# Kernel optimization log

Hardware: AMD Instinct MI355X
Metric: run time of the kernel (lower is better)

Reference implementation:

```python
import jax, jax.numpy as jnp
import numpy as np

NUM_GRAPHS = 1024

def setup_inputs() -> dict:
    key = jax.random.key(0)
    ks = jax.random.split(key, 6)
    N, E = 500000, 16000000
    x = jax.random.normal(ks[0], (N, 4), dtype=jnp.float32)
    edge_index = jax.random.randint(ks[1], (2, E), 0, N, dtype=jnp.int32)
    batch = jnp.sort(jax.random.randint(ks[2], (N,), 0, NUM_GRAPHS, dtype=jnp.int32))
    eps = jnp.zeros((), dtype=jnp.float32)
    W1 = jax.random.normal(ks[3], (4, 16), dtype=jnp.float32) * 0.5
    b1 = jnp.zeros((16,), dtype=jnp.float32)
    W2 = jax.random.normal(ks[4], (16, 4), dtype=jnp.float32) * 0.25
    b2 = jnp.zeros((4,), dtype=jnp.float32)
    return {"x": x, "edge_index": edge_index, "batch": batch,
            "eps": eps, "W1": W1, "b1": b1, "W2": W2, "b2": b2}

def reference(x, edge_index, batch, eps, W1, b1, W2, b2):
    N = x.shape[0]
    src, dst = edge_index[0], edge_index[1]
    # GINConv aggregation: sum of neighbor (source) features at each target node
    agg = jax.ops.segment_sum(x[src], dst, num_segments=N)  # [N, 4]
    h = (1.0 + eps) * x + agg
    # 2-layer MLP: Lin(4,16) -> ReLU -> Lin(16,4)
    h = jax.nn.relu(h @ W1 + b1) @ W2 + b2
    h = jax.nn.relu(h)
    # global_mean_pool over batch segment ids
    sums = jax.ops.segment_sum(h, batch, num_segments=NUM_GRAPHS)      # [G, 4]
    cnts = jax.ops.segment_sum(jnp.ones((N,), h.dtype), batch, num_segments=NUM_GRAPHS)
    pooled = sums / jnp.maximum(cnts, 1.0)[:, None]
    return jax.nn.log_softmax(pooled, axis=1)
```

## Files before the change

### kernel.cpp

```cpp
#include <hip/hip_runtime.h>

#define NUM_GRAPHS 1024
#define BIN_BITS 10
#define BIN_SIZE (1 << BIN_BITS)
#define EB 8192
#define STH 512
#define EPT 16
#define ACCTH 256
#define ACCW 4

typedef int v4i __attribute__((ext_vector_type(4)));

__device__ inline unsigned bf16_rn(float f) {
    unsigned u = __float_as_uint(f);
    return (u + 0x7FFFu + ((u >> 16) & 1u)) >> 16;
}
__global__ void prep_kernel(const float4* __restrict__ x, uint2* __restrict__ x16,
                            int N, int* __restrict__ cursor,
                            float* __restrict__ gsum, float* __restrict__ gcnt,
                            int cap) {
    int i = blockIdx.x * blockDim.x + threadIdx.x;
    if (i < 512) cursor[i] = i * cap;
    if (i < NUM_GRAPHS * 4) gsum[i] = 0.0f;
    if (i < NUM_GRAPHS) gcnt[i] = 0.0f;
    if (i < N) {
        float4 v = x[i];
        uint2 r;
        r.x = bf16_rn(v.x) | (bf16_rn(v.y) << 16);
        r.y = bf16_rn(v.z) | (bf16_rn(v.w) << 16);
        x16[i] = r;
    }
}

__global__ void __launch_bounds__(STH) bin_scatter(const int* __restrict__ src,
                                                   const int* __restrict__ dst,
                                                   int* __restrict__ packed,
                                                   int* __restrict__ cursor,
                                                   int E, int cap, int nb) {
    __shared__ int shist[512];
    __shared__ int sprefix[513];
    __shared__ int sgbase[512];
    __shared__ int spacked[EB];
    __shared__ unsigned short sbin[EB];
    __shared__ int wsum[8];

    const int t = threadIdx.x;
    const int lane = t & 63;
    const int wave = t >> 6;
    const int b0 = blockIdx.x * EB;
    const int myBase = b0 + t * EPT;

    for (int j = t; j < 512; j += STH) shist[j] = 0;
    __syncthreads();

    int pv[EPT];
    int bl[EPT];
    const bool full = (myBase + EPT <= E);
    if (full) {
#pragma unroll
        for (int v = 0; v < EPT / 4; ++v) {
            int4 d = *(const int4*)(dst + myBase + v * 4);
            int4 s = *(const int4*)(src + myBase + v * 4);
            int bn, lp;
            bn = ((unsigned)d.x) >> BIN_BITS; lp = atomicAdd(&shist[bn], 1);
            pv[v * 4 + 0] = ((d.x & (BIN_SIZE - 1)) << 19) | s.x;
            bl[v * 4 + 0] = (bn << 13) | lp;
            bn = ((unsigned)d.y) >> BIN_BITS; lp = atomicAdd(&shist[bn], 1);
            pv[v * 4 + 1] = ((d.y & (BIN_SIZE - 1)) << 19) | s.y;
            bl[v * 4 + 1] = (bn << 13) | lp;
            bn = ((unsigned)d.z) >> BIN_BITS; lp = atomicAdd(&shist[bn], 1);
            pv[v * 4 + 2] = ((d.z & (BIN_SIZE - 1)) << 19) | s.z;
            bl[v * 4 + 2] = (bn << 13) | lp;
            bn = ((unsigned)d.w) >> BIN_BITS; lp = atomicAdd(&shist[bn], 1);
            pv[v * 4 + 3] = ((d.w & (BIN_SIZE - 1)) << 19) | s.w;
            bl[v * 4 + 3] = (bn << 13) | lp;
        }
    } else {
#pragma unroll
        for (int i = 0; i < EPT; ++i) {
            int e = myBase + i;
            bool ok = e < E;
            int d = ok ? dst[e] : 0;
            int s = ok ? src[e] : 0;
            int bn = ((unsigned)d) >> BIN_BITS;
            int lp = 0;
            if (ok) lp = atomicAdd(&shist[bn], 1);
            pv[i] = ((d & (BIN_SIZE - 1)) << 19) | s;
            bl[i] = ok ? ((bn << 13) | lp) : -1;
        }
    }
    __syncthreads();

    {
        int v = shist[t];
        int inc = v;
#pragma unroll
        for (int off = 1; off < 64; off <<= 1) {
            int u = __shfl_up(inc, off);
            if (lane >= off) inc += u;
        }
        if (lane == 63) wsum[wave] = inc;
        __syncthreads();
        if (t == 0) {
            int acc = 0;
#pragma unroll
            for (int w = 0; w < 8; ++w) { int c = wsum[w]; wsum[w] = acc; acc += c; }
        }
        __syncthreads();
        sprefix[t + 1] = inc + wsum[wave];
        if (t == 0) sprefix[0] = 0;
        if (t < nb && v > 0) sgbase[t] = atomicAdd(&cursor[t], v);
    }
    __syncthreads();

    if (full) {
#pragma unroll
        for (int i = 0; i < EPT; ++i) {
            int bn = ((unsigned)bl[i]) >> 13;
            int lp = bl[i] & 0x1FFF;
            int idx = sprefix[bn] + lp;
            spacked[idx] = pv[i];
            sbin[idx] = (unsigned short)bn;
        }
    } else {
#pragma unroll
        for (int i = 0; i < EPT; ++i) {
            if (bl[i] >= 0) {
                int bn = ((unsigned)bl[i]) >> 13;
                int lp = bl[i] & 0x1FFF;
                int idx = sprefix[bn] + lp;
                spacked[idx] = pv[i];
                sbin[idx] = (unsigned short)bn;
            }
        }
    }
    __syncthreads();

    int cnt = sprefix[nb < 512 ? nb : 512];
    int totE = E - b0; if (totE < 0) totE = 0;
    if (cnt > totE) cnt = totE;
    for (int j = t; j < cnt; j += STH) {
        int bn = sbin[j];
        int pos = sgbase[bn] + (j - sprefix[bn]);
        if (pos < (bn + 1) * cap)
            __builtin_nontemporal_store(spacked[j], &packed[pos]);
    }
}

__global__ void __launch_bounds__(ACCTH) bin_accum_mlp_pool(
        const float4* __restrict__ x,
        const uint2* __restrict__ x16,
        const int* __restrict__ packed,
        const int* __restrict__ cursor,
        const int* __restrict__ batch,
        const float* __restrict__ eps_p,
        const float* __restrict__ W1, const float* __restrict__ b1,
        const float* __restrict__ W2, const float* __restrict__ b2,
        float* __restrict__ gsum, float* __restrict__ gcnt,
        int N, int cap) {
    __shared__ float planes[ACCW][BIN_SIZE][4];

    const int bin = blockIdx.x;
    const int t = threadIdx.x;
    const int lane = t & 63;
    const int wave = t >> 6;

    {
        float4* pz = (float4*)&planes[0][0][0];
        float4 z; z.x = 0.f; z.y = 0.f; z.z = 0.f; z.w = 0.f;
#pragma unroll
        for (int i = 0; i < 16; ++i) pz[t + i * ACCTH] = z;
    }
    __syncthreads();

    const int start = bin * cap;
    int end = cursor[bin];
    if (end > start + cap) end = start + cap;
    int cnt = end - start; if (cnt < 0) cnt = 0;

    int seg = ((cnt + ACCW - 1) / ACCW + 3) & ~3;
    int s0 = start + wave * seg;
    int s1 = s0 + seg; if (s1 > end) s1 = end;

    for (int base = s0; base < s1; base += 256) {
        int b = base + lane * 4;
        int pe[4];
        if (b + 3 < s1) {
            v4i p4 = __builtin_nontemporal_load((const v4i*)(packed + b));
            pe[0] = p4.x; pe[1] = p4.y; pe[2] = p4.z; pe[3] = p4.w;
        } else {
            pe[0] = (b + 0 < s1) ? packed[b + 0] : -1;
            pe[1] = (b + 1 < s1) ? packed[b + 1] : -1;
            pe[2] = (b + 2 < s1) ? packed[b + 2] : -1;
            pe[3] = (b + 3 < s1) ? packed[b + 3] : -1;
        }
        uint2 g[4];
#pragma unroll
        for (int k = 0; k < 4; ++k) g[k] = x16[pe[k] & 0x7FFFF];

#pragma unroll
        for (int k = 0; k < 4; ++k) {
            int p = pe[k];
            bool ok = p >= 0;
            int dl = (((unsigned)p) >> 19) & (BIN_SIZE - 1);
            unsigned long long m;
            {
                unsigned long long bv = __ballot(ok);
                m = ok ? bv : ~bv;
#pragma unroll
                for (int bb = 0; bb < BIN_BITS; ++bb) {
                    unsigned long long bl_ = __ballot((dl >> bb) & 1);
                    m &= ((dl >> bb) & 1) ? bl_ : ~bl_;
                }
            }
            int rank = ok ? (int)__popcll(m & ((1ull << lane) - 1ull)) : -1;

            float v0 = __uint_as_float(g[k].x << 16);
            float v1 = __uint_as_float(g[k].x & 0xFFFF0000u);
            float v2 = __uint_as_float(g[k].y << 16);
            float v3 = __uint_as_float(g[k].y & 0xFFFF0000u);
            float4* pp = (float4*)&planes[wave][dl][0];
            for (int pass = 0; __any(rank >= pass); ++pass) {
                if (rank == pass) {
                    float4 a = *pp;
                    a.x += v0; a.y += v1; a.z += v2; a.w += v3;
                    *pp = a;
                }
            }
        }
    }
    __syncthreads();

    const float eps = eps_p[0];
    for (int half = 0; half < 4; ++half) {
        int node = t + half * ACCTH;
        float4 a = *(const float4*)&planes[0][node][0];
#pragma unroll
        for (int w = 1; w < ACCW; ++w) {
            float4 bq = *(const float4*)&planes[w][node][0];
            a.x += bq.x; a.y += bq.y; a.z += bq.z; a.w += bq.w;
        }

        int n = bin * BIN_SIZE + node;
        bool valid = n < N;
        float o0 = 0.f, o1 = 0.f, o2 = 0.f, o3 = 0.f;
        int g = -1;
        if (valid) {
            float4 xv = x[n];
            float h0 = (1.0f + eps) * xv.x + a.x;
            float h1 = (1.0f + eps) * xv.y + a.y;
            float h2 = (1.0f + eps) * xv.z + a.z;
            float h3 = (1.0f + eps) * xv.w + a.w;

            float tmp[16];
#pragma unroll
            for (int j = 0; j < 16; ++j) {
                float v = b1[j] + h0 * W1[j] + h1 * W1[16 + j] + h2 * W1[32 + j] + h3 * W1[48 + j];
                tmp[j] = v > 0.0f ? v : 0.0f;
            }
            float o[4];
#pragma unroll
            for (int j = 0; j < 4; ++j) {
                float v = b2[j];
#pragma unroll
                for (int k = 0; k < 16; ++k) v += tmp[k] * W2[k * 4 + j];
                o[j] = v > 0.0f ? v : 0.0f;
            }
            o0 = o[0]; o1 = o[1]; o2 = o[2]; o3 = o[3];
            g = batch[n];
        }

        int g0 = __shfl(g, 0);
        bool uni = __all(g == g0);
        if (uni && g0 >= 0) {
#pragma unroll
            for (int off = 32; off > 0; off >>= 1) {
                o0 += __shfl_down(o0, off);
                o1 += __shfl_down(o1, off);
                o2 += __shfl_down(o2, off);
                o3 += __shfl_down(o3, off);
            }
            if (lane == 0) {
                unsafeAtomicAdd(&gsum[(size_t)g0 * 4 + 0], o0);
                unsafeAtomicAdd(&gsum[(size_t)g0 * 4 + 1], o1);
                unsafeAtomicAdd(&gsum[(size_t)g0 * 4 + 2], o2);
                unsafeAtomicAdd(&gsum[(size_t)g0 * 4 + 3], o3);
                unsafeAtomicAdd(&gcnt[g0], 64.0f);
            }
        } else if (valid) {
            unsafeAtomicAdd(&gsum[(size_t)g * 4 + 0], o0);
            unsafeAtomicAdd(&gsum[(size_t)g * 4 + 1], o1);
            unsafeAtomicAdd(&gsum[(size_t)g * 4 + 2], o2);
            unsafeAtomicAdd(&gsum[(size_t)g * 4 + 3], o3);
            unsafeAtomicAdd(&gcnt[g], 1.0f);
        }
    }
}

__global__ void pool_softmax_kernel(const float* __restrict__ gsum,
                                    const float* __restrict__ gcnt,
                                    float* __restrict__ out) {
    int g = blockIdx.x * blockDim.x + threadIdx.x;
    if (g >= NUM_GRAPHS) return;
    float c = fmaxf(gcnt[g], 1.0f);
    float p0 = gsum[g * 4 + 0] / c;
    float p1 = gsum[g * 4 + 1] / c;
    float p2 = gsum[g * 4 + 2] / c;
    float p3 = gsum[g * 4 + 3] / c;
    float m = fmaxf(fmaxf(p0, p1), fmaxf(p2, p3));
    float s = expf(p0 - m) + expf(p1 - m) + expf(p2 - m) + expf(p3 - m);
    float lse = m + logf(s);
    out[g * 4 + 0] = p0 - lse;
    out[g * 4 + 1] = p1 - lse;
    out[g * 4 + 2] = p2 - lse;
    out[g * 4 + 3] = p3 - lse;
}

__global__ void edge_scatter_kernel(const float4* __restrict__ x,
                                    const int* __restrict__ src,
                                    const int* __restrict__ dst,
                                    float* __restrict__ agg,
                                    int E) {
    int t = blockIdx.x * blockDim.x + threadIdx.x;
    int e = t * 4;
    if (e + 3 < E) {
        int4 s = *(const int4*)(src + e);
        int4 d = *(const int4*)(dst + e);
        float4 xv;
        xv = x[s.x];
        unsafeAtomicAdd(&agg[(size_t)d.x * 4 + 0], xv.x);
        unsafeAtomicAdd(&agg[(size_t)d.x * 4 + 1], xv.y);
        unsafeAtomicAdd(&agg[(size_t)d.x * 4 + 2], xv.z);
        unsafeAtomicAdd(&agg[(size_t)d.x * 4 + 3], xv.w);
        xv = x[s.y];
        unsafeAtomicAdd(&agg[(size_t)d.y * 4 + 0], xv.x);
        unsafeAtomicAdd(&agg[(size_t)d.y * 4 + 1], xv.y);
        unsafeAtomicAdd(&agg[(size_t)d.y * 4 + 2], xv.z);
        unsafeAtomicAdd(&agg[(size_t)d.y * 4 + 3], xv.w);
        xv = x[s.z];
        unsafeAtomicAdd(&agg[(size_t)d.z * 4 + 0], xv.x);
        unsafeAtomicAdd(&agg[(size_t)d.z * 4 + 1], xv.y);
        unsafeAtomicAdd(&agg[(size_t)d.z * 4 + 2], xv.z);
        unsafeAtomicAdd(&agg[(size_t)d.z * 4 + 3], xv.w);
        xv = x[s.w];
        unsafeAtomicAdd(&agg[(size_t)d.w * 4 + 0], xv.x);
        unsafeAtomicAdd(&agg[(size_t)d.w * 4 + 1], xv.y);
        unsafeAtomicAdd(&agg[(size_t)d.w * 4 + 2], xv.z);
        unsafeAtomicAdd(&agg[(size_t)d.w * 4 + 3], xv.w);
    } else {
        for (int i = e; i < E; ++i) {
            int sv = src[i], dv = dst[i];
            float4 xv = x[sv];
            unsafeAtomicAdd(&agg[(size_t)dv * 4 + 0], xv.x);
            unsafeAtomicAdd(&agg[(size_t)dv * 4 + 1], xv.y);
            unsafeAtomicAdd(&agg[(size_t)dv * 4 + 2], xv.z);
            unsafeAtomicAdd(&agg[(size_t)dv * 4 + 3], xv.w);
        }
    }
}

__global__ void node_mlp_pool_kernel(const float4* __restrict__ x,
                                     const float4* __restrict__ agg,
                                     const int* __restrict__ batch,
                                     const float* __restrict__ eps_p,
                                     const float* __restrict__ W1,
                                     const float* __restrict__ b1,
                                     const float* __restrict__ W2,
                                     const float* __restrict__ b2,
                                     float* __restrict__ gsum,
                                     float* __restrict__ gcnt,
                                     int N) {
    int i = blockIdx.x * blockDim.x + threadIdx.x;
    bool valid = i < N;
    float o0 = 0.f, o1 = 0.f, o2 = 0.f, o3 = 0.f;
    int g = -1;
    if (valid) {
        float eps = eps_p[0];
        float4 xv = x[i];
        float4 av = agg[i];
        float h0 = (1.0f + eps) * xv.x + av.x;
        float h1 = (1.0f + eps) * xv.y + av.y;
        float h2 = (1.0f + eps) * xv.z + av.z;
        float h3 = (1.0f + eps) * xv.w + av.w;
        float tmp[16];
#pragma unroll
        for (int j = 0; j < 16; ++j) {
            float v = b1[j] + h0 * W1[j] + h1 * W1[16 + j] + h2 * W1[32 + j] + h3 * W1[48 + j];
            tmp[j] = v > 0.0f ? v : 0.0f;
        }
        float o[4];
#pragma unroll
        for (int j = 0; j < 4; ++j) {
            float v = b2[j];
#pragma unroll
            for (int k = 0; k < 16; ++k) v += tmp[k] * W2[k * 4 + j];
            o[j] = v > 0.0f ? v : 0.0f;
        }
        o0 = o[0]; o1 = o[1]; o2 = o[2]; o3 = o[3];
        g = batch[i];
    }
    int g0 = __shfl(g, 0);
    bool uni = __all(g == g0);
    if (uni && g0 >= 0) {
#pragma unroll
        for (int off = 32; off > 0; off >>= 1) {
            o0 += __shfl_down(o0, off);
            o1 += __shfl_down(o1, off);
            o2 += __shfl_down(o2, off);
            o3 += __shfl_down(o3, off);
        }
        if ((threadIdx.x & 63) == 0) {
            unsafeAtomicAdd(&gsum[(size_t)g0 * 4 + 0], o0);
            unsafeAtomicAdd(&gsum[(size_t)g0 * 4 + 1], o1);
            unsafeAtomicAdd(&gsum[(size_t)g0 * 4 + 2], o2);
            unsafeAtomicAdd(&gsum[(size_t)g0 * 4 + 3], o3);
            unsafeAtomicAdd(&gcnt[g0], 64.0f);
        }
    } else if (valid) {
        unsafeAtomicAdd(&gsum[(size_t)g * 4 + 0], o0);
        unsafeAtomicAdd(&gsum[(size_t)g * 4 + 1], o1);
        unsafeAtomicAdd(&gsum[(size_t)g * 4 + 2], o2);
        unsafeAtomicAdd(&gsum[(size_t)g * 4 + 3], o3);
        unsafeAtomicAdd(&gcnt[g], 1.0f);
    }
}

extern "C" void kernel_launch(void* const* d_in, const int* in_sizes, int n_in,
                              void* d_out, int out_size, void* d_ws, size_t ws_size,
                              hipStream_t stream) {
    const float* x     = (const float*)d_in[0];
    const int*   ei    = (const int*)d_in[1];
    const int*   batch = (const int*)d_in[2];
    const float* eps   = (const float*)d_in[3];
    const float* W1    = (const float*)d_in[4];
    const float* b1    = (const float*)d_in[5];
    const float* W2    = (const float*)d_in[6];
    const float* b2    = (const float*)d_in[7];

    const int N = in_sizes[0] / 4;
    const int E = in_sizes[1] / 2;
    const int* src = ei;
    const int* dst = ei + (size_t)E;

    const int nb = (N + BIN_SIZE - 1) >> BIN_BITS;
    const int epb = (E + nb - 1) / nb;
    int cap = epb + epb / 8 + 1024;
    cap = (cap + 3) & ~3;

    size_t x16_elems = ((size_t)2 * N + 3) & ~(size_t)3;
    size_t packed_elems = ((size_t)nb * cap + 3) & ~(size_t)3;
    size_t need = (x16_elems + packed_elems + 512 + NUM_GRAPHS * 5) * sizeof(float);

    if (nb <= 512 && N < (1 << 19) && need <= ws_size) {
        uint2* x16    = (uint2*)d_ws;
        int*   packed = (int*)d_ws + x16_elems;
        int*   cursor = packed + packed_elems;
        float* gsum   = (float*)(cursor + 512);
        float* gcnt   = gsum + (size_t)NUM_GRAPHS * 4;

        prep_kernel<<<(N + 511) / 512, 512, 0, stream>>>(
            (const float4*)x, x16, N, cursor, gsum, gcnt, cap);

        int nblocks_e = (E + EB - 1) / EB;
        bin_scatter<<<nblocks_e, STH, 0, stream>>>(src, dst, packed, cursor, E, cap, nb);

        bin_accum_mlp_pool<<<nb, ACCTH, 0, stream>>>(
            (const float4*)x, (const uint2*)x16, packed, cursor, batch, eps,
            W1, b1, W2, b2, gsum, gcnt, N, cap);

        pool_softmax_kernel<<<(NUM_GRAPHS + 255) / 256, 256, 0, stream>>>(
            gsum, gcnt, (float*)d_out);
    } else {
        float* agg  = (float*)d_ws;
        float* gsum = agg + (size_t)N * 4;
        float* gcnt = gsum + (size_t)NUM_GRAPHS * 4;
        size_t zero_bytes = ((size_t)N * 4 + NUM_GRAPHS * 5) * sizeof(float);
        (void)hipMemsetAsync(d_ws, 0, zero_bytes, stream);

        int e4 = (E + 3) / 4;
        edge_scatter_kernel<<<(e4 + 255) / 256, 256, 0, stream>>>(
            (const float4*)x, src, dst, agg, E);

        node_mlp_pool_kernel<<<(N + 255) / 256, 256, 0, stream>>>(
            (const float4*)x, (const float4*)agg, batch, eps, W1, b1, W2, b2,
            gsum, gcnt, N);

        pool_softmax_kernel<<<(NUM_GRAPHS + 255) / 256, 256, 0, stream>>>(
            gsum, gcnt, (float*)d_out);
    }
}
```

Before: 439.0 us.

## Scatter edges directly to global bins, halve block size, pad bin cursors

The binning kernel no longer sorts each block's edges in shared memory via a prefix scan before writing them out. Each edge is now written straight to its global bin slot at cursor base plus its local rank. The edge block size is halved (EPT 16 to 8, EB 8192 to 4096), which doubles the number of blocks and the global cursor atomics. Bin cursors are padded to 16 ints apart so that atomics on different bins do not share a cache line. The aim is to cut shared-memory traffic, syncs and LDS footprint to raise occupancy, at the cost of scattered, less coalesced global stores.

```diff
diff --git a/kernel.cpp b/kernel.cpp
--- a/kernel.cpp
+++ b/kernel.cpp
@@ -3,9 +3,10 @@
 #define NUM_GRAPHS 1024
 #define BIN_BITS 10
 #define BIN_SIZE (1 << BIN_BITS)
-#define EB 8192
+#define EB 4096
 #define STH 512
-#define EPT 16
+#define EPT 8
+#define CURS 16
 #define ACCTH 256
 #define ACCW 4
 
@@ -20,7 +21,7 @@
                             float* __restrict__ gsum, float* __restrict__ gcnt,
                             int cap) {
     int i = blockIdx.x * blockDim.x + threadIdx.x;
-    if (i < 512) cursor[i] = i * cap;
+    if (i < 512) cursor[i * CURS] = i * cap;
     if (i < NUM_GRAPHS * 4) gsum[i] = 0.0f;
     if (i < NUM_GRAPHS) gcnt[i] = 0.0f;
     if (i < N) {
@@ -38,15 +39,9 @@
                                                    int* __restrict__ cursor,
                                                    int E, int cap, int nb) {
     __shared__ int shist[512];
-    __shared__ int sprefix[513];
-    __shared__ int sgbase[512];
-    __shared__ int spacked[EB];
-    __shared__ unsigned short sbin[EB];
-    __shared__ int wsum[8];
+    __shared__ int sgb[512];
 
     const int t = threadIdx.x;
-    const int lane = t & 63;
-    const int wave = t >> 6;
     const int b0 = blockIdx.x * EB;
     const int myBase = b0 + t * EPT;
 
@@ -91,25 +86,9 @@
     }
     __syncthreads();
 
-    {
-        int v = shist[t];
-        int inc = v;
-#pragma unroll
-        for (int off = 1; off < 64; off <<= 1) {
-            int u = __shfl_up(inc, off);
-            if (lane >= off) inc += u;
-        }
-        if (lane == 63) wsum[wave] = inc;
-        __syncthreads();
-        if (t == 0) {
-            int acc = 0;
-#pragma unroll
-            for (int w = 0; w < 8; ++w) { int c = wsum[w]; wsum[w] = acc; acc += c; }
-        }
-        __syncthreads();
-        sprefix[t + 1] = inc + wsum[wave];
-        if (t == 0) sprefix[0] = 0;
-        if (t < nb && v > 0) sgbase[t] = atomicAdd(&cursor[t], v);
+    if (t < nb) {
+        int c = shist[t];
+        sgb[t] = (c > 0) ? atomicAdd(&cursor[t * CURS], c) : 0;
     }
     __syncthreads();
 
@@ -118,9 +97,9 @@
         for (int i = 0; i < EPT; ++i) {
             int bn = ((unsigned)bl[i]) >> 13;
             int lp = bl[i] & 0x1FFF;
-            int idx = sprefix[bn] + lp;
-            spacked[idx] = pv[i];
-            sbin[idx] = (unsigned short)bn;
+            int pos = sgb[bn] + lp;
+            if (pos < (bn + 1) * cap)
+                packed[pos] = pv[i];
         }
     } else {
 #pragma unroll
@@ -128,22 +107,11 @@
             if (bl[i] >= 0) {
                 int bn = ((unsigned)bl[i]) >> 13;
                 int lp = bl[i] & 0x1FFF;
-                int idx = sprefix[bn] + lp;
-                spacked[idx] = pv[i];
-                sbin[idx] = (unsigned short)bn;
-            }
-        }
-    }
-    __syncthreads();
-
-    int cnt = sprefix[nb < 512 ? nb : 512];
-    int totE = E - b0; if (totE < 0) totE = 0;
-    if (cnt > totE) cnt = totE;
-    for (int j = t; j < cnt; j += STH) {
-        int bn = sbin[j];
-        int pos = sgbase[bn] + (j - sprefix[bn]);
-        if (pos < (bn + 1) * cap)
-            __builtin_nontemporal_store(spacked[j], &packed[pos]);
+                int pos = sgb[bn] + lp;
+                if (pos < (bn + 1) * cap)
+                    packed[pos] = pv[i];
+            }
+        }
     }
 }
 
@@ -174,7 +142,7 @@
     __syncthreads();
 
     const int start = bin * cap;
-    int end = cursor[bin];
+    int end = cursor[bin * CURS];
     if (end > start + cap) end = start + cap;
     int cnt = end - start; if (cnt < 0) cnt = 0;
 
@@ -449,13 +417,13 @@
 
     size_t x16_elems = ((size_t)2 * N + 3) & ~(size_t)3;
     size_t packed_elems = ((size_t)nb * cap + 3) & ~(size_t)3;
-    size_t need = (x16_elems + packed_elems + 512 + NUM_GRAPHS * 5) * sizeof(float);
+    size_t need = (x16_elems + packed_elems + 512 * CURS + NUM_GRAPHS * 5) * sizeof(float);
 
     if (nb <= 512 && N < (1 << 19) && need <= ws_size) {
         uint2* x16    = (uint2*)d_ws;
         int*   packed = (int*)d_ws + x16_elems;
         int*   cursor = packed + packed_elems;
-        float* gsum   = (float*)(cursor + 512);
+        float* gsum   = (float*)(cursor + 512 * CURS);
         float* gcnt   = gsum + (size_t)NUM_GRAPHS * 4;
 
         prep_kernel<<<(N + 511) / 512, 512, 0, stream>>>(
```

Result: no change. 441.0 us (+0.5%).
